# Optimization experiments

Measured on AMD Instinct MI355X. Metric: run time of the kernel, lower is better.

The kernel has to match this reference:

```python
import jax, jax.numpy as jnp
import numpy as np
from jax import lax

B, H, W, Q, C = 2, 96, 96, 30000, 64
DIMS = [C * 9 + 4, 256, 256, 256, 256, 3]  # imnet MLP


def setup_inputs() -> dict:
    key = jax.random.key(0)
    ks = jax.random.split(key, 20)
    d = {}
    d["inp"] = jax.random.normal(ks[0], (B, 3, H, W), jnp.float32)
    d["coord"] = jax.random.uniform(ks[1], (B, Q, 2), jnp.float32) * 2.0 - 1.0
    d["cell"] = jax.random.uniform(ks[2], (B, Q, 2), jnp.float32) * (2.0 / 256.0)
    d["conv_w"] = jax.random.normal(ks[3], (C, 3, 3, 3), jnp.float32) * 0.1
    d["conv_b"] = jnp.zeros((C,), jnp.float32)
    for i in range(5):
        fan_in = DIMS[i]
        d[f"w{i}"] = jax.random.normal(ks[4 + i], (DIMS[i], DIMS[i + 1]), jnp.float32) / np.sqrt(fan_in)
        d[f"b{i}"] = jnp.zeros((DIMS[i + 1],), jnp.float32)
    return d


def _liif_forward(inp, coord, cell, conv_w, conv_b, ws, bs):
    # encoder: 3x3 conv + tanh (gen_feat)
    feat = lax.conv_general_dilated(inp, conv_w, (1, 1), "SAME",
                                    dimension_numbers=("NCHW", "OIHW", "NCHW"))
    feat = jnp.tanh(feat + conv_b[None, :, None, None])  # [B,C,H,W]
    b, c, h, w = feat.shape

    # feat_unfold: F.unfold(feat, 3, padding=1) -> [B, C*9, H, W]
    pad = jnp.pad(feat, ((0, 0), (0, 0), (1, 1), (1, 1)))
    patches = jnp.stack([pad[:, :, i:i + h, j:j + w] for i in range(3) for j in range(3)], axis=2)
    fu = patches.reshape(b, c * 9, h, w).transpose(0, 2, 3, 1)  # [B,H,W,9C]

    # local ensemble offsets
    offsets = jnp.array([[-1., -1.], [-1., 1.], [1., -1.], [1., 1.]], jnp.float32)
    rad = jnp.array([1.0 / h, 1.0 / w], jnp.float32)  # 2/r/2
    eps = 1e-6
    ec = coord[None] + (offsets * rad)[:, None, None, :] + eps  # [4,B,Q,2]
    ec = jnp.clip(ec, -1 + 1e-10, 1 - 1e-10)

    # grid_sample nearest, align_corners=False: ix = ((x+1)*size - 1)/2, round
    iy = jnp.clip(jnp.round((ec[..., 0] + 1) * h / 2 - 0.5).astype(jnp.int32), 0, h - 1)
    ix = jnp.clip(jnp.round((ec[..., 1] + 1) * w / 2 - 0.5).astype(jnp.int32), 0, w - 1)
    b_idx = jnp.arange(b)[None, :, None]  # [1,B,1]
    q_feat = fu[b_idx, iy, ix]  # [4,B,Q,9C]

    # feat_coord (make_coord): pixel-center coords in [-1,1]
    yc = (-1.0 + (2.0 * jnp.arange(h, dtype=jnp.float32) + 1.0) / h)
    xc = (-1.0 + (2.0 * jnp.arange(w, dtype=jnp.float32) + 1.0) / w)
    fc = jnp.stack(jnp.meshgrid(yc, xc, indexing="ij"), axis=-1)  # [H,W,2]
    q_coord = fc[iy, ix]  # [4,B,Q,2]

    scale = jnp.array([h, w], jnp.float32)
    rel_coord = (coord[None] - q_coord) * scale  # [4,B,Q,2]
    rel_cell = cell * scale  # [B,Q,2]

    x = jnp.concatenate(
        [q_feat, rel_coord, jnp.broadcast_to(rel_cell[None], rel_coord.shape)], axis=-1)  # [4,B,Q,580]

    # imnet MLP
    for wi, bi in zip(ws[:-1], bs[:-1]):
        x = jax.nn.relu(x @ wi + bi)
    x = x @ ws[-1] + bs[-1]  # [4,B,Q,3]

    areas = jnp.abs(jnp.prod(rel_coord, axis=-1, keepdims=True)) + 1e-9
    areas = areas / jnp.sum(areas, axis=0, keepdims=True)
    areas = areas[::-1]  # swap diagonal ensemble weights

    out = jnp.sum(x * areas, axis=0)  # [B,Q,3]
    return jnp.tanh(out) * 1.01  # fat_tanh(eps=0.01)


def reference(inp, coord, cell, conv_w, conv_b, w0, b0, w1, b1, w2, b2, w3, b3, w4, b4):
    return _liif_forward(inp, coord, cell, conv_w, conv_b,
                         [w0, w1, w2, w3, w4], [b0, b1, b2, b3, b4])
```

## Files before the change

### kernel.cpp

```cpp
#include <hip/hip_runtime.h>


typedef _Float16 half8   __attribute__((ext_vector_type(8)));
typedef _Float16 half4v  __attribute__((ext_vector_type(4)));
typedef _Float16 half2v  __attribute__((ext_vector_type(2)));
typedef float    float4v __attribute__((ext_vector_type(4)));
typedef float    floatx16 __attribute__((ext_vector_type(16)));

__device__ __forceinline__ _Float16 to_h(float v) {
  return (_Float16)fminf(fmaxf(v, -60000.0f), 60000.0f);
}

#define NQ 30000
#define QT 469
#define QTP 472

__global__ void prep_kernel(const float* __restrict__ w0,
                            const float* __restrict__ w1,
                            const float* __restrict__ w2,
                            const float* __restrict__ w3,
                            const float* __restrict__ w4,
                            _Float16* __restrict__ p0, _Float16* __restrict__ p1,
                            _Float16* __restrict__ p2, _Float16* __restrict__ p3,
                            _Float16* __restrict__ p4) {
  int idx = blockIdx.x * 256 + threadIdx.x;
  if (idx < 18944) {
    int kb = idx >> 8, n = idx & 255;
    half8 hv;
#pragma unroll
    for (int i = 0; i < 8; ++i) {
      int f = kb * 8 + i;
      float v = 0.0f;
      if (f < 576)      v = w0[((f & 63) * 9 + (f >> 6)) * 256 + n];
      else if (f < 580) v = w0[f * 256 + n];
      hv[i] = (_Float16)v;
    }
    *(half8*)(p0 + idx * 8) = hv;
  } else if (idx < 43520) {
    int j = idx - 18944;
    int l = j >> 13;
    int j2 = j & 8191;
    int kb = j2 >> 8, n = j2 & 255;
    const float* w = (l == 0) ? w1 : (l == 1) ? w2 : w3;
    _Float16* p = (l == 0) ? p1 : (l == 1) ? p2 : p3;
    half8 hv;
#pragma unroll
    for (int i = 0; i < 8; ++i)
      hv[i] = (_Float16)w[(kb * 8 + i) * 256 + n];
    *(half8*)(p + j2 * 8) = hv;
  } else if (idx < 44032) {
    int j = idx - 43520;
    int kb = j >> 4, n = j & 15;
    half8 hv;
#pragma unroll
    for (int i = 0; i < 8; ++i) {
      float v = (n < 3) ? w4[(kb * 8 + i) * 3 + n] : 0.0f;
      hv[i] = (_Float16)v;
    }
    *(half8*)(p4 + j * 8) = hv;
  }
}

__global__ void conv_kernel(const float* __restrict__ inp,
                            const float* __restrict__ cw,
                            const float* __restrict__ cb,
                            _Float16* __restrict__ P) {
  __shared__ __align__(16) float s_w[1728];
  __shared__ __align__(16) float s_b[64];
  for (int i = threadIdx.x; i < 1728; i += 256) s_w[i] = cw[i];
  if (threadIdx.x < 64) s_b[threadIdx.x] = cb[threadIdx.x];
  __syncthreads();
  int tid = blockIdx.x * 256 + threadIdx.x;
  if (tid >= 2 * 98 * 98) return;
  int b = tid / 9604;
  int rem = tid % 9604;
  int yy = rem / 98, xx = rem % 98;
  alignas(16) _Float16 outv[64];
  if (yy == 0 || yy == 97 || xx == 0 || xx == 97) {
#pragma unroll
    for (int c = 0; c < 64; ++c) outv[c] = (_Float16)0.0f;
  } else {
    int y = yy - 1, x = xx - 1;
    float win[27];
#pragma unroll
    for (int ci = 0; ci < 3; ++ci)
#pragma unroll
      for (int ky = 0; ky < 3; ++ky)
#pragma unroll
        for (int kx = 0; kx < 3; ++kx) {
          int yi = y + ky - 1, xi = x + kx - 1;
          float v = 0.0f;
          if (yi >= 0 && yi < 96 && xi >= 0 && xi < 96)
            v = inp[((b * 3 + ci) * 96 + yi) * 96 + xi];
          win[ci * 9 + ky * 3 + kx] = v;
        }
    for (int co = 0; co < 64; ++co) {
      float acc = s_b[co];
#pragma unroll
      for (int k = 0; k < 27; ++k) acc = fmaf(win[k], s_w[co * 27 + k], acc);
      outv[co] = (_Float16)tanhf(acc);
    }
  }
  _Float16* dst = P + tid * 64;
#pragma unroll
  for (int j = 0; j < 8; ++j) ((half8*)dst)[j] = ((const half8*)outv)[j];
}

__global__ __launch_bounds__(256, 2) void gmat_kernel(
    const _Float16* __restrict__ P,
    const _Float16* __restrict__ wp0,
    _Float16* __restrict__ G) {
  const int t    = threadIdx.x;
  const int lane = t & 63;
  const int wv   = t >> 6;
  const int ln32 = lane & 31;
  const int hi   = lane >> 5;
  const int pb   = blockIdx.x * 128;

  int voffB[4]; int gidx[4];
#pragma unroll
  for (int nt2 = 0; nt2 < 4; ++nt2) {
    int g   = pb + nt2 * 32 + ln32;
    int bb  = g / 9216;
    int rem = g - bb * 9216;
    int ry  = rem / 96;
    int rx  = rem - ry * 96;
    int pix = (bb * 98 + ry) * 98 + rx;
    voffB[nt2] = pix * 128 + hi * 16;
    gidx[nt2]  = pix * 256;
  }
  const char* Pb = (const char*)P;
  const _Float16* wb0 = wp0 + (hi * 256 + wv * 64 + ln32) * 8;

  floatx16 acc[2][4];
#pragma unroll
  for (int mt2 = 0; mt2 < 2; ++mt2)
#pragma unroll
    for (int nt2 = 0; nt2 < 4; ++nt2) acc[mt2][nt2] = (floatx16)(0.0f);

  half8 bfA[4], bfB[4], afA[2], afB[2];
  afA[0] = *(const half8*)(wb0);          afA[1] = *(const half8*)(wb0 + 256);
  afB[0] = *(const half8*)(wb0 + 4096);   afB[1] = *(const half8*)(wb0 + 4096 + 256);
#pragma unroll
  for (int nt2 = 0; nt2 < 4; ++nt2) {
    bfA[nt2] = *(const half8*)(Pb + voffB[nt2]);
    bfB[nt2] = *(const half8*)(Pb + voffB[nt2] + 32);
  }
#pragma unroll 1
  for (int s = 0; s < 36; s += 2) {
#pragma unroll
    for (int mt2 = 0; mt2 < 2; ++mt2)
#pragma unroll
      for (int nt2 = 0; nt2 < 4; ++nt2)
        acc[mt2][nt2] = __builtin_amdgcn_mfma_f32_32x32x16_f16(
            afA[mt2], bfA[nt2], acc[mt2][nt2], 0, 0, 0);
    {
      const int sp = (s + 2 <= 35) ? (s + 2) : 35;
      const int patch = sp >> 2;
      const int off = ((patch / 3) * 98 + (patch % 3)) * 128 + ((sp & 3) << 5);
      afA[0] = *(const half8*)(wb0 + sp * 4096);
      afA[1] = *(const half8*)(wb0 + sp * 4096 + 256);
#pragma unroll
      for (int nt2 = 0; nt2 < 4; ++nt2)
        bfA[nt2] = *(const half8*)(Pb + voffB[nt2] + off);
    }
#pragma unroll
    for (int mt2 = 0; mt2 < 2; ++mt2)
#pragma unroll
      for (int nt2 = 0; nt2 < 4; ++nt2)
        acc[mt2][nt2] = __builtin_amdgcn_mfma_f32_32x32x16_f16(
            afB[mt2], bfB[nt2], acc[mt2][nt2], 0, 0, 0);
    {
      const int sp = (s + 3 <= 35) ? (s + 3) : 35;
      const int patch = sp >> 2;
      const int off = ((patch / 3) * 98 + (patch % 3)) * 128 + ((sp & 3) << 5);
      afB[0] = *(const half8*)(wb0 + sp * 4096);
      afB[1] = *(const half8*)(wb0 + sp * 4096 + 256);
#pragma unroll
      for (int nt2 = 0; nt2 < 4; ++nt2)
        bfB[nt2] = *(const half8*)(Pb + voffB[nt2] + off);
    }
  }
#pragma unroll
  for (int mt2 = 0; mt2 < 2; ++mt2)
#pragma unroll
    for (int nt2 = 0; nt2 < 4; ++nt2) {
      half8 c0, c1;
#pragma unroll
      for (int j = 0; j < 8; ++j) {
        c0[j] = (_Float16)acc[mt2][nt2][j];
        c1[j] = (_Float16)acc[mt2][nt2][8 + j];
      }
      _Float16* ga = G + gidx[nt2] + (wv * 2 + mt2) * 32 + hi * 16;
      *(half8*)(ga)     = c0;
      *(half8*)(ga + 8) = c1;
    }
}

__device__ __forceinline__ void writeback32(floatx16 (&acc)[2][4],
                                            const float* __restrict__ sb,
                                            _Float16 (*s_h)[264],
                                            int wv, int ln32, int hi) {
#pragma unroll
  for (int mt2 = 0; mt2 < 2; ++mt2) {
    const int mb = wv * 64 + mt2 * 32 + 4 * hi;
#pragma unroll
    for (int g = 0; g < 4; ++g) {
      const int m0 = mb + 8 * g;
      float b0 = sb[m0], b1 = sb[m0 + 1], b2 = sb[m0 + 2], b3 = sb[m0 + 3];
#pragma unroll
      for (int nt2 = 0; nt2 < 4; ++nt2) {
        const int n = nt2 * 32 + ln32;
        float v0 = fmaxf(acc[mt2][nt2][4 * g + 0] + b0, 0.0f);
        float v1 = fmaxf(acc[mt2][nt2][4 * g + 1] + b1, 0.0f);
        float v2 = fmaxf(acc[mt2][nt2][4 * g + 2] + b2, 0.0f);
        float v3 = fmaxf(acc[mt2][nt2][4 * g + 3] + b3, 0.0f);
        half2v lo  = __builtin_bit_cast(half2v, __builtin_amdgcn_cvt_pkrtz(v0, v1));
        half2v hi2 = __builtin_bit_cast(half2v, __builtin_amdgcn_cvt_pkrtz(v2, v3));
        half4v hv;
        hv[0] = lo[0]; hv[1] = lo[1]; hv[2] = hi2[0]; hv[3] = hi2[1];
        *(half4v*)(&s_h[n][m0]) = hv;
      }
    }
  }
}

__device__ __forceinline__ void layer256(const _Float16* __restrict__ wbl,
                                         _Float16 (*s_h)[264],
                                         int ln32, int hi,
                                         floatx16 (&acc)[2][4]) {
#pragma unroll
  for (int mt2 = 0; mt2 < 2; ++mt2)
#pragma unroll
    for (int nt2 = 0; nt2 < 4; ++nt2) acc[mt2][nt2] = (floatx16)(0.0f);
  half8 afA[2], afB[2], bfA[4], bfB[4];
  afA[0] = *(const half8*)(wbl);
  afA[1] = *(const half8*)(wbl + 256);
  afB[0] = *(const half8*)(wbl + 4096);
  afB[1] = *(const half8*)(wbl + 4096 + 256);
#pragma unroll
  for (int nt2 = 0; nt2 < 4; ++nt2) {
    bfA[nt2] = *(const half8*)(&s_h[nt2 * 32 + ln32][hi * 8]);
    bfB[nt2] = *(const half8*)(&s_h[nt2 * 32 + ln32][16 + hi * 8]);
  }
#pragma unroll 1
  for (int s = 0; s < 16; s += 2) {
#pragma unroll
    for (int mt2 = 0; mt2 < 2; ++mt2)
#pragma unroll
      for (int nt2 = 0; nt2 < 4; ++nt2)
        acc[mt2][nt2] = __builtin_amdgcn_mfma_f32_32x32x16_f16(
            afA[mt2], bfA[nt2], acc[mt2][nt2], 0, 0, 0);
    {
      const int sc = (s + 2 < 16) ? (s + 2) : 0;
      const int sw = (s + 2 < 16) ? (s + 2) : 15;
      afA[0] = *(const half8*)(wbl + sw * 4096);
      afA[1] = *(const half8*)(wbl + sw * 4096 + 256);
#pragma unroll
      for (int nt2 = 0; nt2 < 4; ++nt2)
        bfA[nt2] = *(const half8*)(&s_h[nt2 * 32 + ln32][sc * 16 + hi * 8]);
    }
#pragma unroll
    for (int mt2 = 0; mt2 < 2; ++mt2)
#pragma unroll
      for (int nt2 = 0; nt2 < 4; ++nt2)
        acc[mt2][nt2] = __builtin_amdgcn_mfma_f32_32x32x16_f16(
            afB[mt2], bfB[nt2], acc[mt2][nt2], 0, 0, 0);
    {
      const int sc = (s + 3 < 16) ? (s + 3) : 0;
      const int sw = (s + 3 < 16) ? (s + 3) : 15;
      afB[0] = *(const half8*)(wbl + sw * 4096);
      afB[1] = *(const half8*)(wbl + sw * 4096 + 256);
#pragma unroll
      for (int nt2 = 0; nt2 < 4; ++nt2)
        bfB[nt2] = *(const half8*)(&s_h[nt2 * 32 + ln32][sc * 16 + hi * 8]);
    }
  }
}

__global__ __launch_bounds__(256, 2) void liif_main(
    const float* __restrict__ coord, const float* __restrict__ cell,
    const float* __restrict__ bias0, const float* __restrict__ bias1,
    const float* __restrict__ bias2, const float* __restrict__ bias3,
    const float* __restrict__ bias4,
    const _Float16* __restrict__ G,
    const _Float16* __restrict__ wp0, const _Float16* __restrict__ wp1,
    const _Float16* __restrict__ wp2, const _Float16* __restrict__ wp3,
    const _Float16* __restrict__ wp4,
    float* __restrict__ out) {
  __shared__ __align__(16) int      s_pix[4][64];
  __shared__ __align__(16) float    s_area[4][64];
  __shared__ __align__(16) _Float16 s_ext[4][64][8];
  __shared__ __align__(16) float    s_bias[1028];
  __shared__ __align__(16) float    s_out[128][4];
  __shared__ __align__(16) float    s_num[64][4];
  __shared__ __align__(16) _Float16 s_h[128][264];

  const int t   = threadIdx.x;
  const int blk = blockIdx.x;
  const int bb  = (blk & 4) >> 2;
  const int tile = (blk >> 3) * 4 + (blk & 3);
  const int q0  = tile * 64;

  for (int i = t; i < 1027; i += 256) {
    float v;
    if (i < 256)       v = bias0[i];
    else if (i < 512)  v = bias1[i - 256];
    else if (i < 768)  v = bias2[i - 512];
    else if (i < 1024) v = bias3[i - 768];
    else               v = bias4[i - 1024];
    s_bias[i] = v;
  }

  if (t < 64) {
    int q = q0 + t;
    bool valid = q < NQ;
    float c0 = 0.f, c1 = 0.f, e0 = 0.f, e1 = 0.f;
    if (valid) {
      int base = (bb * NQ + q) * 2;
      c0 = coord[base]; c1 = coord[base + 1];
      e0 = cell[base];  e1 = cell[base + 1];
    }
    float rc0 = e0 * 96.0f, rc1 = e1 * 96.0f;
#pragma unroll
    for (int o = 0; o < 4; ++o) {
      float oy = (o < 2) ? -1.0f : 1.0f;
      float ox = (o & 1) ? 1.0f : -1.0f;
      float ec0 = (c0 + oy * (1.0f / 96.0f)) + 1e-6f;
      float ec1 = (c1 + ox * (1.0f / 96.0f)) + 1e-6f;
      ec0 = fminf(fmaxf(ec0, -1.0f), 1.0f);
      ec1 = fminf(fmaxf(ec1, -1.0f), 1.0f);
      int iy = (int)rintf(((ec0 + 1.0f) * 96.0f) * 0.5f - 0.5f);
      int ix = (int)rintf(((ec1 + 1.0f) * 96.0f) * 0.5f - 0.5f);
      iy = min(max(iy, 0), 95); ix = min(max(ix, 0), 95);
      float qc0 = -1.0f + (2.0f * (float)iy + 1.0f) / 96.0f;
      float qc1 = -1.0f + (2.0f * (float)ix + 1.0f) / 96.0f;
      float r0 = (c0 - qc0) * 96.0f;
      float r1 = (c1 - qc1) * 96.0f;
      s_pix[o][t]  = (bb * 98 + iy) * 98 + ix;
      s_area[o][t] = fabsf(r0 * r1) + 1e-9f;
      s_ext[o][t][0] = to_h(r0);  s_ext[o][t][1] = to_h(r1);
      s_ext[o][t][2] = to_h(rc0); s_ext[o][t][3] = to_h(rc1);
      s_ext[o][t][4] = (_Float16)0.0f; s_ext[o][t][5] = (_Float16)0.0f;
      s_ext[o][t][6] = (_Float16)0.0f; s_ext[o][t][7] = (_Float16)0.0f;
    }
    s_num[t][0] = 0.f; s_num[t][1] = 0.f; s_num[t][2] = 0.f; s_num[t][3] = 0.f;
  }
  __syncthreads();

  const int lane = t & 63;
  const int wv   = t >> 6;
  const int ln32 = lane & 31;
  const int hi   = lane >> 5;
  const int ln16 = lane & 15;
  const int lg   = lane >> 4;

  const _Float16* wb0 = wp0 + (hi * 256 + wv * 64 + ln32) * 8;
  const _Float16* wb1 = wp1 + (hi * 256 + wv * 64 + ln32) * 8;
  const _Float16* wb2 = wp2 + (hi * 256 + wv * 64 + ln32) * 8;
  const _Float16* wb3 = wp3 + (hi * 256 + wv * 64 + ln32) * 8;

#pragma unroll 1
  for (int p = 0; p < 2; ++p) {
    int pixr[4]; int eidx[4];
#pragma unroll
    for (int nt2 = 0; nt2 < 4; ++nt2) {
      int r = nt2 * 32 + ln32;
      int o = p * 2 + (r >> 6);
      int q = r & 63;
      pixr[nt2] = s_pix[o][q];
      eidx[nt2] = (o * 64 + q) * 8;
    }

    floatx16 acc[2][4];
#pragma unroll
    for (int mt2 = 0; mt2 < 2; ++mt2)
#pragma unroll
      for (int nt2 = 0; nt2 < 4; ++nt2) {
        const _Float16* ga = G + pixr[nt2] * 256 + (wv * 2 + mt2) * 32 + hi * 16;
        half8 g0 = *(const half8*)(ga);
        half8 g1 = *(const half8*)(ga + 8);
        floatx16 a;
#pragma unroll
        for (int j = 0; j < 8; ++j) {
          a[j]     = (float)g0[j];
          a[8 + j] = (float)g1[j];
        }
        acc[mt2][nt2] = a;
      }
    {
      half8 ae[2];
      ae[0] = *(const half8*)(wb0 + 36 * 4096);
      ae[1] = *(const half8*)(wb0 + 36 * 4096 + 256);
      half8 z = {(_Float16)0, (_Float16)0, (_Float16)0, (_Float16)0,
                 (_Float16)0, (_Float16)0, (_Float16)0, (_Float16)0};
      half8 bfe[4];
#pragma unroll
      for (int nt2 = 0; nt2 < 4; ++nt2)
        bfe[nt2] = (hi == 0) ? *(const half8*)(&s_ext[0][0][0] + eidx[nt2]) : z;
#pragma unroll
      for (int mt2 = 0; mt2 < 2; ++mt2)
#pragma unroll
        for (int nt2 = 0; nt2 < 4; ++nt2)
          acc[mt2][nt2] = __builtin_amdgcn_mfma_f32_32x32x16_f16(
              ae[mt2], bfe[nt2], acc[mt2][nt2], 0, 0, 0);
    }
    writeback32(acc, s_bias, s_h, wv, ln32, hi);
    __syncthreads();

    layer256(wb1, s_h, ln32, hi, acc);
    __syncthreads();
    writeback32(acc, s_bias + 256, s_h, wv, ln32, hi);
    __syncthreads();

    layer256(wb2, s_h, ln32, hi, acc);
    __syncthreads();
    writeback32(acc, s_bias + 512, s_h, wv, ln32, hi);
    __syncthreads();

    layer256(wb3, s_h, ln32, hi, acc);
    __syncthreads();
    writeback32(acc, s_bias + 768, s_h, wv, ln32, hi);
    __syncthreads();

    half8 af4 = *(const half8*)(wp4 + (lg * 16 + ln16) * 8);
    float4v a4[2];
    a4[0] = (float4v){0.f, 0.f, 0.f, 0.f};
    a4[1] = (float4v){0.f, 0.f, 0.f, 0.f};
#pragma unroll 1
    for (int s = 0; s < 8; ++s) {
      half8 afc = af4;
      if (s < 7)
        af4 = *(const half8*)(wp4 + (((s + 1) * 4 + lg) * 16 + ln16) * 8);
#pragma unroll
      for (int u = 0; u < 2; ++u) {
        int row = (2 * wv + u) * 16 + ln16;
        half8 bf = *(const half8*)(&s_h[row][s * 32 + lg * 8]);
        a4[u] = __builtin_amdgcn_mfma_f32_16x16x32_f16(afc, bf, a4[u], 0, 0, 0);
      }
    }
    if (lg == 0) {
#pragma unroll
      for (int u = 0; u < 2; ++u) {
        int row = (2 * wv + u) * 16 + ln16;
        *(float4v*)(&s_out[row][0]) = a4[u];
      }
    }
    __syncthreads();

    if (t < 64) {
      float a_lo = s_area[3 - 2 * p][t];
      float a_hi = s_area[2 - 2 * p][t];
#pragma unroll
      for (int j = 0; j < 3; ++j)
        s_num[t][j] += s_out[t][j] * a_lo + s_out[64 + t][j] * a_hi;
    }
  }

  if (t < 64) {
    int q = q0 + t;
    if (q < NQ) {
      float den = s_area[0][t] + s_area[1][t] + s_area[2][t] + s_area[3][t];
      int ob = (bb * NQ + q) * 3;
#pragma unroll
      for (int j = 0; j < 3; ++j) {
        float v = s_num[t][j] / den + s_bias[1024 + j];
        out[ob + j] = tanhf(v) * 1.01f;
      }
    }
  }
}

extern "C" void kernel_launch(void* const* d_in, const int* in_sizes, int n_in,
                              void* d_out, int out_size, void* d_ws, size_t ws_size,
                              hipStream_t stream) {
  const float* inp   = (const float*)d_in[0];
  const float* coord = (const float*)d_in[1];
  const float* cell  = (const float*)d_in[2];
  const float* cw    = (const float*)d_in[3];
  const float* cb    = (const float*)d_in[4];
  const float* w0    = (const float*)d_in[5];
  const float* b0    = (const float*)d_in[6];
  const float* w1    = (const float*)d_in[7];
  const float* b1    = (const float*)d_in[8];
  const float* w2    = (const float*)d_in[9];
  const float* b2    = (const float*)d_in[10];
  const float* w3    = (const float*)d_in[11];
  const float* b3    = (const float*)d_in[12];
  const float* w4    = (const float*)d_in[13];
  const float* b4    = (const float*)d_in[14];

  char* ws = (char*)d_ws;
  _Float16* P   = (_Float16*)(ws);
  _Float16* wp0 = (_Float16*)(ws + 2458624);
  _Float16* wp1 = (_Float16*)(ws + 2761728);
  _Float16* wp2 = (_Float16*)(ws + 2892800);
  _Float16* wp3 = (_Float16*)(ws + 3023872);
  _Float16* wp4 = (_Float16*)(ws + 3154944);
  _Float16* G   = (_Float16*)(ws + 3163136);
  float* outp = (float*)d_out;

  hipLaunchKernelGGL(prep_kernel, dim3(172), dim3(256), 0, stream,
                     w0, w1, w2, w3, w4, wp0, wp1, wp2, wp3, wp4);
  hipLaunchKernelGGL(conv_kernel, dim3(76), dim3(256), 0, stream, inp, cw, cb, P);
  hipLaunchKernelGGL(gmat_kernel, dim3(144), dim3(256), 0, stream, P, wp0, G);
  hipLaunchKernelGGL(liif_main, dim3(8 * (QTP / 4)), dim3(256), 0, stream,
                     coord, cell, b0, b1, b2, b3, b4,
                     G, wp0, wp1, wp2, wp3, wp4, outp);
}
```

Baseline: 268.5 us.

## Stage padded feature rows in LDS for gmat and tile one image row per block

```diff
diff --git a/kernel.cpp b/kernel.cpp
--- a/kernel.cpp
+++ b/kernel.cpp
@@ -106,92 +106,96 @@
   for (int j = 0; j < 8; ++j) ((half8*)dst)[j] = ((const half8*)outv)[j];
 }
 
-__global__ __launch_bounds__(256, 2) void gmat_kernel(
+__global__ __launch_bounds__(256, 1) void gmat_kernel(
     const _Float16* __restrict__ P,
     const _Float16* __restrict__ wp0,
     _Float16* __restrict__ G) {
+  __shared__ __align__(16) _Float16 s_p[3][98][68];
+
   const int t    = threadIdx.x;
   const int lane = t & 63;
   const int wv   = t >> 6;
   const int ln32 = lane & 31;
   const int hi   = lane >> 5;
-  const int pb   = blockIdx.x * 128;
-
-  int voffB[4]; int gidx[4];
-#pragma unroll
-  for (int nt2 = 0; nt2 < 4; ++nt2) {
-    int g   = pb + nt2 * 32 + ln32;
-    int bb  = g / 9216;
-    int rem = g - bb * 9216;
-    int ry  = rem / 96;
-    int rx  = rem - ry * 96;
-    int pix = (bb * 98 + ry) * 98 + rx;
-    voffB[nt2] = pix * 128 + hi * 16;
-    gidx[nt2]  = pix * 256;
-  }
-  const char* Pb = (const char*)P;
+  const int blk  = blockIdx.x;
+  const int bb   = (blk & 4) >> 2;
+  const int y    = (blk >> 3) * 4 + (blk & 3);
+
+  const int rowbase = (bb * 98 + y) * 98 * 64;
+  for (int j = t; j < 2352; j += 256) {
+    int row = j / 784;
+    int jr  = j - row * 784;
+    int px  = jr >> 3;
+    int ci  = jr & 7;
+    half8 v = *(const half8*)(P + rowbase + row * 6272 + jr * 8);
+    *(half8*)(&s_p[row][px][ci * 8]) = v;
+  }
+  __syncthreads();
+
   const _Float16* wb0 = wp0 + (hi * 256 + wv * 64 + ln32) * 8;
 
-  floatx16 acc[2][4];
+  floatx16 acc[2][3];
 #pragma unroll
   for (int mt2 = 0; mt2 < 2; ++mt2)
 #pragma unroll
-    for (int nt2 = 0; nt2 < 4; ++nt2) acc[mt2][nt2] = (floatx16)(0.0f);
-
-  half8 bfA[4], bfB[4], afA[2], afB[2];
+    for (int nt = 0; nt < 3; ++nt) acc[mt2][nt] = (floatx16)(0.0f);
+
+  half8 afA[2], afB[2];
   afA[0] = *(const half8*)(wb0);          afA[1] = *(const half8*)(wb0 + 256);
   afB[0] = *(const half8*)(wb0 + 4096);   afB[1] = *(const half8*)(wb0 + 4096 + 256);
-#pragma unroll
-  for (int nt2 = 0; nt2 < 4; ++nt2) {
-    bfA[nt2] = *(const half8*)(Pb + voffB[nt2]);
-    bfB[nt2] = *(const half8*)(Pb + voffB[nt2] + 32);
-  }
+
 #pragma unroll 1
   for (int s = 0; s < 36; s += 2) {
-#pragma unroll
-    for (int mt2 = 0; mt2 < 2; ++mt2)
-#pragma unroll
-      for (int nt2 = 0; nt2 < 4; ++nt2)
-        acc[mt2][nt2] = __builtin_amdgcn_mfma_f32_32x32x16_f16(
-            afA[mt2], bfA[nt2], acc[mt2][nt2], 0, 0, 0);
     {
+      const int patch = s >> 2;
+      const int py = patch / 3, px = patch % 3;
+      const int cb = ((s & 3) << 4) + hi * 8;
+      half8 bf[3];
+#pragma unroll
+      for (int nt = 0; nt < 3; ++nt)
+        bf[nt] = *(const half8*)(&s_p[py][nt * 32 + ln32 + px][cb]);
+#pragma unroll
+      for (int mt2 = 0; mt2 < 2; ++mt2)
+#pragma unroll
+        for (int nt = 0; nt < 3; ++nt)
+          acc[mt2][nt] = __builtin_amdgcn_mfma_f32_32x32x16_f16(
+              afA[mt2], bf[nt], acc[mt2][nt], 0, 0, 0);
       const int sp = (s + 2 <= 35) ? (s + 2) : 35;
-      const int patch = sp >> 2;
-      const int off = ((patch / 3) * 98 + (patch % 3)) * 128 + ((sp & 3) << 5);
       afA[0] = *(const half8*)(wb0 + sp * 4096);
       afA[1] = *(const half8*)(wb0 + sp * 4096 + 256);
-#pragma unroll
-      for (int nt2 = 0; nt2 < 4; ++nt2)
-        bfA[nt2] = *(const half8*)(Pb + voffB[nt2] + off);
-    }
-#pragma unroll
-    for (int mt2 = 0; mt2 < 2; ++mt2)
-#pragma unroll
-      for (int nt2 = 0; nt2 < 4; ++nt2)
-        acc[mt2][nt2] = __builtin_amdgcn_mfma_f32_32x32x16_f16(
-            afB[mt2], bfB[nt2], acc[mt2][nt2], 0, 0, 0);
+    }
     {
+      const int s1 = s + 1;
+      const int patch = s1 >> 2;
+      const int py = patch / 3, px = patch % 3;
+      const int cb = ((s1 & 3) << 4) + hi * 8;
+      half8 bf[3];
+#pragma unroll
+      for (int nt = 0; nt < 3; ++nt)
+        bf[nt] = *(const half8*)(&s_p[py][nt * 32 + ln32 + px][cb]);
+#pragma unroll
+      for (int mt2 = 0; mt2 < 2; ++mt2)
+#pragma unroll
+        for (int nt = 0; nt < 3; ++nt)
+          acc[mt2][nt] = __builtin_amdgcn_mfma_f32_32x32x16_f16(
+              afB[mt2], bf[nt], acc[mt2][nt], 0, 0, 0);
       const int sp = (s + 3 <= 35) ? (s + 3) : 35;
-      const int patch = sp >> 2;
-      const int off = ((patch / 3) * 98 + (patch % 3)) * 128 + ((sp & 3) << 5);
       afB[0] = *(const half8*)(wb0 + sp * 4096);
       afB[1] = *(const half8*)(wb0 + sp * 4096 + 256);
-#pragma unroll
-      for (int nt2 = 0; nt2 < 4; ++nt2)
-        bfB[nt2] = *(const half8*)(Pb + voffB[nt2] + off);
-    }
-  }
+    }
+  }
+  const int gybase = ((bb * 98 + y) * 98) * 256;
 #pragma unroll
   for (int mt2 = 0; mt2 < 2; ++mt2)
 #pragma unroll
-    for (int nt2 = 0; nt2 < 4; ++nt2) {
+    for (int nt = 0; nt < 3; ++nt) {
       half8 c0, c1;
 #pragma unroll
       for (int j = 0; j < 8; ++j) {
-        c0[j] = (_Float16)acc[mt2][nt2][j];
-        c1[j] = (_Float16)acc[mt2][nt2][8 + j];
+        c0[j] = (_Float16)acc[mt2][nt][j];
+        c1[j] = (_Float16)acc[mt2][nt][8 + j];
       }
-      _Float16* ga = G + gidx[nt2] + (wv * 2 + mt2) * 32 + hi * 16;
+      _Float16* ga = G + gybase + (nt * 32 + ln32) * 256 + (wv * 2 + mt2) * 32 + hi * 16;
       *(half8*)(ga)     = c0;
       *(half8*)(ga + 8) = c1;
     }
@@ -503,7 +507,7 @@
   hipLaunchKernelGGL(prep_kernel, dim3(172), dim3(256), 0, stream,
                      w0, w1, w2, w3, w4, wp0, wp1, wp2, wp3, wp4);
   hipLaunchKernelGGL(conv_kernel, dim3(76), dim3(256), 0, stream, inp, cw, cb, P);
-  hipLaunchKernelGGL(gmat_kernel, dim3(144), dim3(256), 0, stream, P, wp0, G);
+  hipLaunchKernelGGL(gmat_kernel, dim3(192), dim3(256), 0, stream, P, wp0, G);
   hipLaunchKernelGGL(liif_main, dim3(8 * (QTP / 4)), dim3(256), 0, stream,
                      coord, cell, b0, b1, b2, b3, b4,
                      G, wp0, wp1, wp2, wp3, wp4, outp);
```

Result: no change. 264.4 us (-1.5%).
